# Kernel optimization log

Measured on AMD Instinct MI355X. Metric: run time of the kernel, lower is better.

## Reference

```python
import jax, jax.numpy as jnp
import numpy as np

B = 4096          # batch_size
D_EMB = 16        # per-side embedding dim (embed_to_from width = 2*D_EMB)
D_HIGH = 784      # flattened high-dim feature size
NSR = 5           # negative_sample_rate
A = 1.576943      # UMAP _a
B_PARAM = 0.8950608  # UMAP _b
REPULSION = 1.0
EPS = 1e-4
GLOBAL_LOSS = 0.5
TOTAL_STEPS = 1000
BATCH_COUNT = 500  # fixed step for deterministic alpha/beta
WARMUP = int(0.05 * TOTAL_STEPS)


def _safe_sqrt(sq):
    # sqrt with zero (not NaN) gradient at 0, matching zero-distance pairs
    safe = jnp.where(sq > 0, sq, 1.0)
    return jnp.where(sq > 0, jnp.sqrt(safe), 0.0)


def _pairwise_dist(x):
    # ||x_i - x_j|| via gram trick; avoids materializing [N,N,D]
    sq = jnp.sum(x * x, axis=1)                      # [N]
    gram = x @ x.T                                   # [N,N]
    d2 = sq[:, None] + sq[None, :] - 2.0 * gram
    return _safe_sqrt(jnp.maximum(d2, 0.0))


def _umap_ce_loss(embed_to_from, perm):
    e_to, e_from = jnp.split(embed_to_from, 2, axis=1)   # [B, D_EMB] each
    neg_to = jnp.repeat(e_to, NSR, axis=0)               # [B*NSR, D_EMB]
    repeat_neg = jnp.repeat(e_from, NSR, axis=0)
    neg_from = repeat_neg[perm]                          # shuffled negatives
    d_pos = _safe_sqrt(jnp.sum((e_to - e_from) ** 2, axis=1))
    d_neg = _safe_sqrt(jnp.sum((neg_to - neg_from) ** 2, axis=1))
    dist = jnp.concatenate([d_pos, d_neg], axis=0)       # [B*(1+NSR)]
    p_dist = 1.0 / (1.0 + A * dist ** (2.0 * B_PARAM))
    p_graph = jnp.concatenate([jnp.ones(B, p_dist.dtype), jnp.zeros(B * NSR, p_dist.dtype)])
    attraction = -p_graph * jnp.log(jnp.clip(p_dist, EPS, 1.0))
    repellant = -(1.0 - p_graph) * jnp.log(jnp.clip(1.0 - p_dist, EPS, 1.0)) * REPULSION
    return jnp.mean(attraction + repellant)


def _global_feature_loss(embed_to_from, to_x):
    e_to = embed_to_from[:, :D_EMB]
    to_x = to_x.reshape(to_x.shape[0], -1)
    high_dis = _pairwise_dist(to_x)     # [N,N]
    low_dis = _pairwise_dist(e_to)      # [N,N]
    # row-wise pearson correlation between high_dis and low_dis
    h = high_dis - jnp.mean(high_dis, axis=1, keepdims=True)
    l = low_dis - jnp.mean(low_dis, axis=1, keepdims=True)
    num = jnp.sum(h * l, axis=1)
    den = jnp.sqrt(jnp.sum(h * h, axis=1)) * jnp.sqrt(jnp.sum(l * l, axis=1))
    corr = jnp.mean(num / den)
    return -corr


def _alpha_beta():
    if BATCH_COUNT >= WARMUP:
        if BATCH_COUNT <= 0.9 * TOTAL_STEPS:
            beta = max(0.0, GLOBAL_LOSS * (1 - BATCH_COUNT / (TOTAL_STEPS - WARMUP * 4)) ** 2)
        else:
            beta = 0.0
        alpha = max(0.0, 1 - beta)
    else:
        alpha = 0.0
        beta = GLOBAL_LOSS
    return alpha, beta


def setup_inputs() -> dict:
    key = jax.random.key(0)
    k1, k2, k3 = jax.random.split(key, 3)
    embed_to_from = jax.random.normal(k1, (B, 2 * D_EMB), dtype=jnp.float32)
    placeholder = jax.random.normal(k2, (B, D_HIGH), dtype=jnp.float32)
    perm = jax.random.permutation(k3, B * NSR).astype(jnp.int32)
    return {"embed_to_from": embed_to_from, "placeholder": placeholder, "perm": perm}


def reference(embed_to_from, placeholder, perm):
    loss = _umap_ce_loss(embed_to_from, perm)
    loss_g = _global_feature_loss(embed_to_from, placeholder)
    alpha, beta = _alpha_beta()
    return alpha * loss + beta * loss_g
```

## Files before the change

### kernel.cpp

```cpp
#include <hip/hip_runtime.h>
#include <hip/hip_bf16.h>
#include <math.h>

#define NB    4096
#define DH    784
#define NSR   5
#define NNEG  (NB*NSR)
#define NTOT  (NB + NNEG)

#define A_CONST 1.576943f
#define PEXP    1.7901216f
#define EPS_C   1.0e-4f
#define ALPHA_C 0.9296875f
#define BETA_C  0.0703125f

#define NBLK  528
#define BUFB  8192
#define CH    262144

typedef __hip_bfloat16 bf16;
typedef short bf16x8 __attribute__((ext_vector_type(8)));
typedef float f32x4  __attribute__((ext_vector_type(4)));
typedef float f32x2  __attribute__((ext_vector_type(2)));
typedef long long2v __attribute__((ext_vector_type(2)));

#define WS_XF8    0
#define WS_EBF    3407872
#define WS_SQX    3670016
#define WS_SQE    3686400
#define WS_ACC5   3702784
#define WS_UPART  8945664
#define WS_CNT    8946304

__device__ __forceinline__ void gl2lds16(const void* g, void* l) {
    __builtin_amdgcn_global_load_lds(
        (const __attribute__((address_space(1))) unsigned int*)g,
        (__attribute__((address_space(3))) unsigned int*)l,
        16, 0, 0);
}

__global__ void prep_fused(const float* __restrict__ X, const float* __restrict__ emb,
                           const int* __restrict__ perm, unsigned char* __restrict__ Xf8,
                           float* __restrict__ sqx, bf16* __restrict__ Ebf,
                           float* __restrict__ sqe, float* __restrict__ upart,
                           float* __restrict__ acc5, unsigned* __restrict__ cnt) {
    if (blockIdx.x == 0 && threadIdx.x == 0) *cnt = 0u;
    if (blockIdx.x < 1024) {
        const int wave = threadIdx.x >> 6, lane = threadIdx.x & 63;
        const int row = blockIdx.x * 4 + wave;
        const float4* xr = (const float4*)(X + (size_t)row * DH);
        int* xb = (int*)Xf8;
        float s = 0.f;
        #pragma unroll
        for (int it = 0; it < 4; ++it) {
            const int idx = lane + it * 64;
            if (idx < 208) {
                const int c = idx >> 4, p = idx & 15;
                const int q = p >> 2, h = (p >> 1) & 1, w = p & 1;
                const int src = c * 16 + h * 8 + q * 2 + w;
                int pk = 0;
                if (src < 196) {
                    float4 v = xr[src];
                    s += v.x * v.x + v.y * v.y + v.z * v.z + v.w * v.w;
                    int lo = __builtin_amdgcn_cvt_pk_fp8_f32(v.x, v.y, 0, false);
                    pk = __builtin_amdgcn_cvt_pk_fp8_f32(v.z, v.w, lo, true);
                }
                xb[(size_t)c * 65536 + (size_t)row * 16 + p] = pk;
            }
        }
        #pragma unroll
        for (int off = 32; off; off >>= 1) s += __shfl_down(s, off, 64);
        if (lane == 0) sqx[row] = s;
        return;
    }
    const int ub = blockIdx.x - 1024;
    const int t = ub * 256 + threadIdx.x;
    if (t < 5 * NB) acc5[t] = 0.f;
    float val = 0.f;
    if (t < NB) {
        const float4* av = (const float4*)(emb + (size_t)t * 32);
        float4 t0 = av[0], t1 = av[1], t2 = av[2], t3 = av[3];
        float4 f0 = av[4], f1 = av[5], f2 = av[6], f3 = av[7];
        bf16* eb = Ebf + (size_t)t * 32;
        union { bf16 h[4]; ushort4 u; } cv;
        #define ST4(dst, q) cv.h[0]=__float2bfloat16(q.x); cv.h[1]=__float2bfloat16(q.y); \
                            cv.h[2]=__float2bfloat16(q.z); cv.h[3]=__float2bfloat16(q.w); \
                            *(ushort4*)(dst) = cv.u;
        ST4(eb,      t0) ST4(eb + 4,  t1) ST4(eb + 8,  t2) ST4(eb + 12, t3)
        #undef ST4
        ushort4 z = {0, 0, 0, 0};
        *(ushort4*)(eb + 16) = z; *(ushort4*)(eb + 20) = z;
        *(ushort4*)(eb + 24) = z; *(ushort4*)(eb + 28) = z;
        sqe[t] = t0.x*t0.x + t0.y*t0.y + t0.z*t0.z + t0.w*t0.w
               + t1.x*t1.x + t1.y*t1.y + t1.z*t1.z + t1.w*t1.w
               + t2.x*t2.x + t2.y*t2.y + t2.z*t2.z + t2.w*t2.w
               + t3.x*t3.x + t3.y*t3.y + t3.z*t3.z + t3.w*t3.w;
        float d2 = 0.f;
        #define D2(a, b) { float4 df = {a.x-b.x, a.y-b.y, a.z-b.z, a.w-b.w}; \
                           d2 += df.x*df.x + df.y*df.y + df.z*df.z + df.w*df.w; }
        D2(t0, f0) D2(t1, f1) D2(t2, f2) D2(t3, f3)
        #undef D2
        float d = sqrtf(d2);
        float p = 1.f / (1.f + A_CONST * powf(d, PEXP));
        val = -logf(fminf(fmaxf(p, EPS_C), 1.f));
    } else if (t < NTOT) {
        const int k = t - NB;
        const int ti = k / 5;
        const int fi = perm[k] / 5;
        const float4* at = (const float4*)(emb + (size_t)ti * 32);
        const float4* bt = (const float4*)(emb + (size_t)fi * 32 + 16);
        float d2 = 0.f;
        #pragma unroll
        for (int q = 0; q < 4; ++q) {
            float4 a = at[q], b = bt[q];
            float4 df = {a.x-b.x, a.y-b.y, a.z-b.z, a.w-b.w};
            d2 += df.x*df.x + df.y*df.y + df.z*df.z + df.w*df.w;
        }
        float d = sqrtf(d2);
        float p = 1.f / (1.f + A_CONST * powf(d, PEXP));
        val = -logf(fminf(fmaxf(1.f - p, EPS_C), 1.f));
    }
    #pragma unroll
    for (int off = 32; off; off >>= 1) val += __shfl_down(val, off, 64);
    __shared__ float ps[4];
    if ((threadIdx.x & 63) == 0) ps[threadIdx.x >> 6] = val;
    __syncthreads();
    if (threadIdx.x == 0) upart[ub] = ps[0] + ps[1] + ps[2] + ps[3];
}

__global__ __launch_bounds__(512, 4) void gram_kernel(
    const unsigned char* __restrict__ Xf8, const bf16* __restrict__ Ebf,
    const float* __restrict__ sqx, const float* __restrict__ sqe,
    float* __restrict__ acc5, const float* __restrict__ upart,
    unsigned* __restrict__ cnt, float* __restrict__ out) {
    __shared__ __align__(16) unsigned char smem[67584];
    unsigned char* As = smem;
    unsigned char* Bs = smem + 4 * BUFB;
    float* sqxs = (float*)(smem + 65536);
    float* sqes = (float*)(smem + 66560);
    float* scr  = (float*)smem;

    int bi, bj;
    {
        const int k = blockIdx.x & 7;
        const int idx = blockIdx.x >> 3;
        int g = -1, r = 0;
        if (k < 6) {
            const int SG[6] = {0,0,0,1,1,2}, SH[6] = {1,2,3,2,3,3};
            if (idx < 64) { bi = SG[k]*8 + (idx>>3); bj = SH[k]*8 + (idx&7); }
            else {
                const int DG[6] = {1,0,3,1,3,3};
                const int DR[6] = {32,34,30,34,32,34};
                g = DG[k]; r = DR[k] + (idx - 64);
            }
        } else if (k == 6) {
            if (idx < 34) { g = 0; r = idx; } else { g = 1; r = idx - 34; }
        } else {
            if (idx < 36) { g = 2; r = idx; } else { g = 3; r = idx - 36; }
        }
        if (g >= 0) {
            int a = 0;
            while (r >= 8 - a) { r -= 8 - a; ++a; }
            bi = g * 8 + a; bj = g * 8 + a + r;
        }
    }
    const int i0 = bi * 128, j0 = bj * 128;

    const int tid  = threadIdx.x;
    const int wave = tid >> 6;
    const int lane = tid & 63;
    const int wy = wave >> 1, wx = wave & 1;
    const int quad = lane >> 4, l15 = lane & 15;

    f32x4 acc[2][4];
    #pragma unroll
    for (int a = 0; a < 2; ++a)
        #pragma unroll
        for (int b = 0; b < 4; ++b)
            acc[a][b] = (f32x4){0.f, 0.f, 0.f, 0.f};

    const int rA  = lane >> 2;
    const int gsb = (((lane & 3) ^ ((lane >> 3) & 3))) * 16;
    const unsigned char* gA = Xf8 + (size_t)(i0 + wave * 16 + rA) * 64 + gsb;
    const unsigned char* gB = Xf8 + (size_t)(j0 + wave * 16 + rA) * 64 + gsb;

    if (tid < 128) {
        sqxs[tid] = sqx[i0 + tid]; sqxs[128 + tid] = sqx[j0 + tid];
        sqes[tid] = sqe[i0 + tid]; sqes[128 + tid] = sqe[j0 + tid];
    }
    __syncthreads();

    #pragma unroll
    for (int s = 0; s < 3; ++s) {
        gl2lds16(gA, As + s * BUFB + wave * 1024);
        gl2lds16(gB, Bs + s * BUFB + wave * 1024);
        gA += CH; gB += CH;
    }

    const int key = (l15 >> 1) & 3;
    const int boX = ((quad ^ key) << 4);

    #pragma unroll
    for (int t = 0; t < 13; ++t) {
        if (t < 12) { asm volatile("s_waitcnt vmcnt(4)" ::: "memory"); }
        else        { asm volatile("s_waitcnt vmcnt(2)" ::: "memory"); }
        __builtin_amdgcn_s_barrier();
        const int cur = (t & 3) * BUFB;
        const int nb  = ((t + 3) & 3) * BUFB;
        if (t < 10) {
            gl2lds16(gA, As + nb + wave * 1024);
            gl2lds16(gB, Bs + nb + wave * 1024);
            gA += CH; gB += CH;
        } else if (t == 10) {
            gl2lds16((const unsigned char*)(Ebf + (size_t)(i0 + wave * 16 + rA) * 32) + gsb,
                     As + BUFB + wave * 1024);
            gl2lds16((const unsigned char*)(Ebf + (size_t)(j0 + wave * 16 + rA) * 32) + gsb,
                     Bs + BUFB + wave * 1024);
        }
        long2v aF[2], bF[4];
        #pragma unroll
        for (int mi = 0; mi < 2; ++mi)
            aF[mi] = *(const long2v*)&As[cur + (wy * 32 + mi * 16 + l15) * 64 + boX];
        #pragma unroll
        for (int ni = 0; ni < 4; ++ni)
            bF[ni] = *(const long2v*)&Bs[cur + (wx * 64 + ni * 16 + l15) * 64 + boX];
        #pragma unroll
        for (int mi = 0; mi < 2; ++mi)
            #pragma unroll
            for (int ni = 0; ni < 4; ++ni) {
                acc[mi][ni] = __builtin_amdgcn_mfma_f32_16x16x32_fp8_fp8(
                    aF[mi][0], bF[ni][0], acc[mi][ni], 0, 0, 0);
                acc[mi][ni] = __builtin_amdgcn_mfma_f32_16x16x32_fp8_fp8(
                    aF[mi][1], bF[ni][1], acc[mi][ni], 0, 0, 0);
            }
    }
    asm volatile("s_waitcnt vmcnt(0)" ::: "memory");
    __builtin_amdgcn_s_barrier();

    bf16x8 afE[2], bfrE[4];
    #pragma unroll
    for (int mi = 0; mi < 2; ++mi)
        afE[mi] = *(const bf16x8*)&As[BUFB + (wy * 32 + mi * 16 + l15) * 64 + boX];
    #pragma unroll
    for (int ni = 0; ni < 4; ++ni)
        bfrE[ni] = *(const bf16x8*)&Bs[BUFB + (wx * 64 + ni * 16 + l15) * 64 + boX];
    float sqxj[4], sqej[4];
    #pragma unroll
    for (int ni = 0; ni < 4; ++ni) {
        const int jl = wx * 64 + ni * 16 + l15;
        sqxj[ni] = sqxs[128 + jl]; sqej[ni] = sqes[128 + jl];
    }
    __syncthreads();

    float cst[4][5];
    #pragma unroll
    for (int ni = 0; ni < 4; ++ni)
        #pragma unroll
        for (int c = 0; c < 5; ++c) cst[ni][c] = 0.f;

    #pragma unroll
    for (int mi = 0; mi < 2; ++mi) {
        f32x4 aE[4];
        #pragma unroll
        for (int ni = 0; ni < 4; ++ni) {
            f32x4 z = (f32x4){0.f, 0.f, 0.f, 0.f};
            aE[ni] = __builtin_amdgcn_mfma_f32_16x16x32_bf16(afE[mi], bfrE[ni], z, 0, 0, 0);
        }
        const int ilb = wy * 32 + mi * 16 + quad * 4;
        float sqxi[4], sqei[4];
        #pragma unroll
        for (int r = 0; r < 4; ++r) { sqxi[r] = sqxs[ilb + r]; sqei[r] = sqes[ilb + r]; }
        float rs[5][4];
        #pragma unroll
        for (int c = 0; c < 5; ++c)
            #pragma unroll
            for (int r = 0; r < 4; ++r) rs[c][r] = 0.f;
        #pragma unroll
        for (int ni = 0; ni < 4; ++ni) {
            const int j = j0 + wx * 64 + ni * 16 + l15;
            #pragma unroll
            for (int r = 0; r < 4; ++r) {
                const int i = i0 + ilb + r;
                float H, L;
                if (i == j) { H = 0.f; L = 0.f; }
                else {
                    float d2  = sqxi[r] + sqxj[ni] - 2.0f * acc[mi][ni][r];
                    H = sqrtf(fmaxf(d2, 0.f));
                    float d2e = sqei[r] + sqej[ni] - 2.0f * aE[ni][r];
                    L = sqrtf(fmaxf(d2e, 0.f));
                }
                rs[0][r] += H; rs[1][r] += H * H; rs[2][r] += L;
                rs[3][r] += L * L; rs[4][r] += H * L;
                cst[ni][0] += H; cst[ni][1] += H * H; cst[ni][2] += L;
                cst[ni][3] += L * L; cst[ni][4] += H * L;
            }
        }
        #pragma unroll
        for (int c = 0; c < 5; ++c)
            #pragma unroll
            for (int r = 0; r < 4; ++r)
                scr[(size_t)((((wx * 5 + c) << 6) + (wy << 4) + (quad << 2) + r)) * 18 + l15]
                    = rs[c][r];
        __syncthreads();
        for (int o = tid; o < 320; o += 512) {
            const int c = o >> 6, li = o & 63;
            const float* p0 = scr + (size_t)((c << 6) + li) * 18;
            const float* p1 = scr + (size_t)(((5 + c) << 6) + li) * 18;
            float s = 0.f;
            #pragma unroll
            for (int k = 0; k < 16; k += 2) {
                f32x2 v0 = *(const f32x2*)&p0[k]; s += v0.x + v0.y;
                f32x2 v1 = *(const f32x2*)&p1[k]; s += v1.x + v1.y;
            }
            const int iloc = ((li >> 4) << 5) + mi * 16 + (li & 15);
            unsafeAtomicAdd(&acc5[(size_t)c * NB + (i0 + iloc)], s);
        }
        __syncthreads();
    }

    if (bi != bj) {
        #pragma unroll
        for (int ni = 0; ni < 4; ++ni) {
            const int jl = wx * 64 + ni * 16 + l15;
            #pragma unroll
            for (int c = 0; c < 5; ++c)
                scr[(size_t)(c * 128 + jl) * 17 + (wy << 2) + quad] = cst[ni][c];
        }
        __syncthreads();
        for (int o = tid; o < 640; o += 512) {
            const int c = o >> 7, j = o & 127;
            const float* p = scr + (size_t)(c * 128 + j) * 17;
            float s = (((p[0] + p[1]) + (p[2] + p[3])) + ((p[4] + p[5]) + (p[6] + p[7])))
                    + (((p[8] + p[9]) + (p[10] + p[11])) + ((p[12] + p[13]) + (p[14] + p[15])));
            unsafeAtomicAdd(&acc5[(size_t)c * NB + (j0 + j)], s);
        }
    }

    __shared__ int lastFlag;
    __syncthreads();
    if (tid == 0) {
        __threadfence();
        lastFlag = (atomicAdd(cnt, 1u) == (unsigned)(NBLK - 1));
    }
    __syncthreads();
    if (lastFlag) {
        __threadfence();
        const float invN = 1.0f / (float)NB;
        float v = 0.f;
        #pragma unroll
        for (int rr = 0; rr < 8; ++rr) {
            const int r = tid + rr * 512;
            const float a  = acc5[0 * NB + r];
            const float b  = acc5[1 * NB + r];
            const float c2 = acc5[2 * NB + r];
            const float d  = acc5[3 * NB + r];
            const float e  = acc5[4 * NB + r];
            float num = e - a * c2 * invN;
            float vh  = fmaxf(b - a * a * invN, 0.f);
            float vl  = fmaxf(d - c2 * c2 * invN, 0.f);
            v += num / (sqrtf(vh) * sqrtf(vl));
        }
        v *= (-BETA_C * invN);
        if (tid < 96) v += upart[tid] * (ALPHA_C / (float)NTOT);
        #pragma unroll
        for (int off = 32; off; off >>= 1) v += __shfl_down(v, off, 64);
        float* fin = (float*)smem;
        __syncthreads();
        if ((tid & 63) == 0) fin[tid >> 6] = v;
        __syncthreads();
        if (tid == 0)
            out[0] = ((fin[0] + fin[1]) + (fin[2] + fin[3]))
                   + ((fin[4] + fin[5]) + (fin[6] + fin[7]));
    }
}

extern "C" void kernel_launch(void* const* d_in, const int* in_sizes, int n_in,
                              void* d_out, int out_size, void* d_ws, size_t ws_size,
                              hipStream_t stream) {
    const float* emb  = (const float*)d_in[0];
    const float* ph   = (const float*)d_in[1];
    const int*   perm = (const int*)d_in[2];
    float* out = (float*)d_out;

    char* ws = (char*)d_ws;
    unsigned char* Xf8 = (unsigned char*)(ws + WS_XF8);
    bf16*  Ebf    = (bf16*) (ws + WS_EBF);
    float* sqx    = (float*)(ws + WS_SQX);
    float* sqe    = (float*)(ws + WS_SQE);
    float* acc5   = (float*)(ws + WS_ACC5);
    float* upart  = (float*)(ws + WS_UPART);
    unsigned* cnt = (unsigned*)(ws + WS_CNT);

    prep_fused<<<1120, 256, 0, stream>>>(ph, emb, perm, Xf8, sqx, Ebf, sqe, upart, acc5, cnt);
    gram_kernel<<<NBLK, 512, 0, stream>>>(Xf8, Ebf, sqx, sqe, acc5, upart, cnt, out);
}
```

Measured before the change: 108.0 us.

## Restructure fp8 gram K-loop into double-buffered two-chunk stages

```diff
diff --git a/kernel.cpp b/kernel.cpp
--- a/kernel.cpp
+++ b/kernel.cpp
@@ -15,8 +15,8 @@
 #define BETA_C  0.0703125f
 
 #define NBLK  528
-#define BUFB  8192
 #define CH    262144
+#define SBUF  32768
 
 typedef __hip_bfloat16 bf16;
 typedef short bf16x8 __attribute__((ext_vector_type(8)));
@@ -134,8 +134,6 @@
     float* __restrict__ acc5, const float* __restrict__ upart,
     unsigned* __restrict__ cnt, float* __restrict__ out) {
     __shared__ __align__(16) unsigned char smem[67584];
-    unsigned char* As = smem;
-    unsigned char* Bs = smem + 4 * BUFB;
     float* sqxs = (float*)(smem + 65536);
     float* sqes = (float*)(smem + 66560);
     float* scr  = (float*)smem;
@@ -183,6 +181,8 @@
     const int gsb = (((lane & 3) ^ ((lane >> 3) & 3))) * 16;
     const unsigned char* gA = Xf8 + (size_t)(i0 + wave * 16 + rA) * 64 + gsb;
     const unsigned char* gB = Xf8 + (size_t)(j0 + wave * 16 + rA) * 64 + gsb;
+    const unsigned char* eA = (const unsigned char*)Ebf + (size_t)(i0 + wave * 16 + rA) * 64 + gsb;
+    const unsigned char* eB = (const unsigned char*)Ebf + (size_t)(j0 + wave * 16 + rA) * 64 + gsb;
 
     if (tid < 128) {
         sqxs[tid] = sqx[i0 + tid]; sqxs[128 + tid] = sqx[j0 + tid];
@@ -190,60 +190,85 @@
     }
     __syncthreads();
 
-    #pragma unroll
-    for (int s = 0; s < 3; ++s) {
-        gl2lds16(gA, As + s * BUFB + wave * 1024);
-        gl2lds16(gB, Bs + s * BUFB + wave * 1024);
-        gA += CH; gB += CH;
-    }
+#define STAGE_X(b, s) { \
+        unsigned char* d = smem + (b) * SBUF + wave * 1024; \
+        gl2lds16(gA + (size_t)(2 * (s)) * CH,     d); \
+        gl2lds16(gA + (size_t)(2 * (s) + 1) * CH, d + 8192); \
+        gl2lds16(gB + (size_t)(2 * (s)) * CH,     d + 16384); \
+        gl2lds16(gB + (size_t)(2 * (s) + 1) * CH, d + 24576); }
+#define STAGE_LAST(b) { \
+        unsigned char* d = smem + (b) * SBUF + wave * 1024; \
+        gl2lds16(gA + (size_t)12 * CH, d); \
+        gl2lds16(eA,                   d + 8192); \
+        gl2lds16(gB + (size_t)12 * CH, d + 16384); \
+        gl2lds16(eB,                   d + 24576); }
+
+    STAGE_X(0, 0)
+    STAGE_X(1, 1)
 
     const int key = (l15 >> 1) & 3;
     const int boX = ((quad ^ key) << 4);
-
-    #pragma unroll
-    for (int t = 0; t < 13; ++t) {
-        if (t < 12) { asm volatile("s_waitcnt vmcnt(4)" ::: "memory"); }
-        else        { asm volatile("s_waitcnt vmcnt(2)" ::: "memory"); }
+    const int aro = (wy * 32 + l15) * 64 + boX;
+    const int bro = (wx * 64 + l15) * 64 + boX;
+
+    #pragma unroll
+    for (int t = 0; t < 7; ++t) {
+        if (t < 6) { asm volatile("s_waitcnt vmcnt(4)" ::: "memory"); }
+        else       { asm volatile("s_waitcnt vmcnt(0)" ::: "memory"); }
         __builtin_amdgcn_s_barrier();
-        const int cur = (t & 3) * BUFB;
-        const int nb  = ((t + 3) & 3) * BUFB;
-        if (t < 10) {
-            gl2lds16(gA, As + nb + wave * 1024);
-            gl2lds16(gB, Bs + nb + wave * 1024);
-            gA += CH; gB += CH;
-        } else if (t == 10) {
-            gl2lds16((const unsigned char*)(Ebf + (size_t)(i0 + wave * 16 + rA) * 32) + gsb,
-                     As + BUFB + wave * 1024);
-            gl2lds16((const unsigned char*)(Ebf + (size_t)(j0 + wave * 16 + rA) * 32) + gsb,
-                     Bs + BUFB + wave * 1024);
-        }
-        long2v aF[2], bF[4];
+        const unsigned char* bb = smem + (t & 1) * SBUF;
+        long2v aF0[2], bF0[4], aF1[2], bF1[4];
         #pragma unroll
         for (int mi = 0; mi < 2; ++mi)
-            aF[mi] = *(const long2v*)&As[cur + (wy * 32 + mi * 16 + l15) * 64 + boX];
+            aF0[mi] = *(const long2v*)&bb[aro + mi * 1024];
         #pragma unroll
         for (int ni = 0; ni < 4; ++ni)
-            bF[ni] = *(const long2v*)&Bs[cur + (wx * 64 + ni * 16 + l15) * 64 + boX];
+            bF0[ni] = *(const long2v*)&bb[16384 + bro + ni * 1024];
+        if (t < 6) {
+            #pragma unroll
+            for (int mi = 0; mi < 2; ++mi)
+                aF1[mi] = *(const long2v*)&bb[8192 + aro + mi * 1024];
+            #pragma unroll
+            for (int ni = 0; ni < 4; ++ni)
+                bF1[ni] = *(const long2v*)&bb[24576 + bro + ni * 1024];
+        }
+        if (t < 5) {
+            asm volatile("s_waitcnt lgkmcnt(0)" ::: "memory");
+            __builtin_amdgcn_s_barrier();
+            if (t < 4) { STAGE_X(t & 1, t + 2) }
+            else       { STAGE_LAST(0) }
+        }
         #pragma unroll
         for (int mi = 0; mi < 2; ++mi)
             #pragma unroll
             for (int ni = 0; ni < 4; ++ni) {
                 acc[mi][ni] = __builtin_amdgcn_mfma_f32_16x16x32_fp8_fp8(
-                    aF[mi][0], bF[ni][0], acc[mi][ni], 0, 0, 0);
+                    aF0[mi][0], bF0[ni][0], acc[mi][ni], 0, 0, 0);
                 acc[mi][ni] = __builtin_amdgcn_mfma_f32_16x16x32_fp8_fp8(
-                    aF[mi][1], bF[ni][1], acc[mi][ni], 0, 0, 0);
+                    aF0[mi][1], bF0[ni][1], acc[mi][ni], 0, 0, 0);
             }
-    }
-    asm volatile("s_waitcnt vmcnt(0)" ::: "memory");
-    __builtin_amdgcn_s_barrier();
+        if (t < 6) {
+            #pragma unroll
+            for (int mi = 0; mi < 2; ++mi)
+                #pragma unroll
+                for (int ni = 0; ni < 4; ++ni) {
+                    acc[mi][ni] = __builtin_amdgcn_mfma_f32_16x16x32_fp8_fp8(
+                        aF1[mi][0], bF1[ni][0], acc[mi][ni], 0, 0, 0);
+                    acc[mi][ni] = __builtin_amdgcn_mfma_f32_16x16x32_fp8_fp8(
+                        aF1[mi][1], bF1[ni][1], acc[mi][ni], 0, 0, 0);
+                }
+        }
+    }
+#undef STAGE_X
+#undef STAGE_LAST
 
     bf16x8 afE[2], bfrE[4];
     #pragma unroll
     for (int mi = 0; mi < 2; ++mi)
-        afE[mi] = *(const bf16x8*)&As[BUFB + (wy * 32 + mi * 16 + l15) * 64 + boX];
+        afE[mi] = *(const bf16x8*)&smem[8192 + aro + mi * 1024];
     #pragma unroll
     for (int ni = 0; ni < 4; ++ni)
-        bfrE[ni] = *(const bf16x8*)&Bs[BUFB + (wx * 64 + ni * 16 + l15) * 64 + boX];
+        bfrE[ni] = *(const bf16x8*)&smem[24576 + bro + ni * 1024];
     float sqxj[4], sqej[4];
     #pragma unroll
     for (int ni = 0; ni < 4; ++ni) {
```

Result: no change. 107.6 us (-0.4%).
